# Kernel optimization log

Measured on AMD Instinct MI355X. Metric: run time of the kernel, lower is better.

## Reference

```python
import jax, jax.numpy as jnp
import numpy as np

D_IN = 256
H = 512
DT = 0.01
LN_EPS = 1e-5


def setup_inputs() -> dict:
    key = jax.random.key(0)
    ks = jax.random.split(key, 12)
    def lin(k, fan_in, shape):
        bound = 1.0 / np.sqrt(fan_in)
        return jax.random.uniform(k, shape, jnp.float32, -bound, bound)
    x = jax.random.normal(ks[0], (64, 1024, D_IN), jnp.float32)
    return {
        "x": x,
        # input_mapper: Linear(D_IN+H, 2H)
        "Wm": lin(ks[1], D_IN + H, (D_IN + H, 2 * H)),
        "bm": lin(ks[2], D_IN + H, (2 * H,)),
        # f_theta: Linear(H,H) -> SiLU -> Linear(H,H)
        "Wf1": lin(ks[3], H, (H, H)),
        "bf1": lin(ks[4], H, (H,)),
        "Wf2": lin(ks[5], H, (H, H)),
        "bf2": lin(ks[6], H, (H,)),
        # tau_net: Linear(H,H) -> Softplus
        "Wt": lin(ks[7], H, (H, H)),
        "bt": lin(ks[8], H, (H,)),
        # LayerNorm(H)
        "gamma": jnp.ones((H,), jnp.float32),
        "beta": jnp.zeros((H,), jnp.float32),
    }


def _layernorm(h, gamma, beta):
    mu = jnp.mean(h, axis=-1, keepdims=True)
    var = jnp.var(h, axis=-1, keepdims=True)
    return (h - mu) * jax.lax.rsqrt(var + LN_EPS) * gamma + beta


def reference(x, Wm, bm, Wf1, bf1, Wf2, bf2, Wt, bt, gamma, beta):
    B = x.shape[0]
    h0 = jnp.zeros((B, H), x.dtype)

    def step(h, u_t):
        combined = jnp.concatenate([u_t, h], axis=-1)      # (B, D_IN+H)
        mapped = combined @ Wm + bm                        # (B, 2H)
        g, core = jnp.split(mapped, 2, axis=-1)
        g = jax.nn.sigmoid(g)
        tau = jax.nn.softplus(core @ Wt + bt) + 1e-6       # (B, H)
        z = g * jnp.tanh(core)
        f = jax.nn.silu(z @ Wf1 + bf1) @ Wf2 + bf2         # (B, H)
        h_new = _layernorm(h + (DT / tau) * f, gamma, beta)
        return h_new, h_new

    # scan over time: x (B,T,D) -> (T,B,D)
    _, hs = jax.lax.scan(step, h0, jnp.swapaxes(x, 0, 1))
    return jnp.swapaxes(hs, 0, 1)                          # (B, T, H)
```

## Files before the change

kernel.cpp:

```cpp
#include <hip/hip_runtime.h>
#include <hip/hip_bf16.h>

typedef unsigned int        u32;
typedef unsigned short      u16;
typedef unsigned long long  u64;

#define T_STEPS 1024
#define NTH     1024
#define NSL     8
#define NGRP    32

#define OFF_WM4   0
#define OFF_WT4   786432
#define OFF_WF14  1048576
#define OFF_WF24  1310720
#define OFF_FLAGS 1572864
#define OFF_XC    1576960
#define XC_ZC 0
#define XC_F1 32768
#define XC_V  49152
#define XC_SQ 65536

__device__ __forceinline__ float bf2f(u16 u){
  union { u32 u; float f; } x; x.u = ((u32)u) << 16; return x.f;
}
__device__ __forceinline__ u32 f2bf_bits(float f){
  union { float f; u32 u; } x; x.f = f;
  u32 u = x.u;
  return ((u + 0x7fffu + ((u >> 16) & 1u)) >> 16) & 0xffffu;
}
__device__ __forceinline__ u32 pack2(float lo, float hi){
  return (f2bf_bits(hi) << 16) | f2bf_bits(lo);
}
__device__ __forceinline__ void split2(float f0, float f1, u32& hi, u32& lo){
  u32 b0 = f2bf_bits(f0), b1 = f2bf_bits(f1);
  hi = (b1 << 16) | b0;
  float r0 = f0 - bf2f((u16)b0);
  float r1 = f1 - bf2f((u16)b1);
  lo = pack2(r0, r1);
}
__device__ __forceinline__ float dot2bf(u32 a, u32 b, float c){
  float d;
  asm("v_dot2_f32_bf16 %0, %1, %2, %3" : "=v"(d) : "v"(a), "v"(b), "v"(c));
  return d;
}
__device__ __forceinline__ float sigmoidf_(float x){ return 1.f/(1.f + __expf(-x)); }
__device__ __forceinline__ float tanhf_(float x){ return 1.f - 2.f/(__expf(2.f*x) + 1.f); }
__device__ __forceinline__ float softplusf_(float x){ return (x > 20.f) ? x : log1pf(__expf(x)); }

__device__ __forceinline__ int sniff_bf16(const void* gamma){
  return (((const u32*)gamma)[0] == 0x3F803F80u) ? 1 : 0;
}
__device__ __forceinline__ float ldsc(const void* p, int i, int isbf){
  return isbf ? bf2f(((const u16*)p)[i]) : ((const float*)p)[i];
}
__device__ __forceinline__ float ldwf(const void* p, long i, int isbf){
  return isbf ? bf2f(((const u16*)p)[i]) : ((const float*)p)[i];
}

__device__ __forceinline__ void xst(u64* p, u32 hi, u32 lo){
  u64 v = ((u64)lo << 32) | (u64)hi;
  __hip_atomic_store(p, v, __ATOMIC_RELAXED, __HIP_MEMORY_SCOPE_AGENT);
}
__device__ __forceinline__ void xst64(u64* p, u64 v){
  __hip_atomic_store(p, v, __ATOMIC_RELAXED, __HIP_MEMORY_SCOPE_AGENT);
}
__device__ __forceinline__ u64 xld(const u64* p){
  return __hip_atomic_load(p, __ATOMIC_RELAXED, __HIP_MEMORY_SCOPE_AGENT);
}

__device__ __forceinline__ void groupsync(u32* line, int j, u32 tgt, u32* deadf)
{
  __syncthreads();
  if (threadIdx.x == 0 && *deadf == 0u) {
    __hip_atomic_store(line + j, tgt, __ATOMIC_RELAXED, __HIP_MEMORY_SCOPE_AGENT);
    u32 gu = 0;
    for (;;) {
      u32 mn = 0xffffffffu;
      #pragma unroll
      for (int q = 0; q < NSL; ++q)
        mn = min(mn, __hip_atomic_load(line + q, __ATOMIC_RELAXED, __HIP_MEMORY_SCOPE_AGENT));
      if (mn >= tgt) break;
      if (++gu > 1000000u) { *deadf = 1u; break; }
      if (gu > 64u) __builtin_amdgcn_s_sleep(1);
    }
  }
  __syncthreads();
}

__global__ void repack_kernel(const void* __restrict__ Wm, const void* __restrict__ Wt,
                              const void* __restrict__ Wf1, const void* __restrict__ Wf2,
                              const void* __restrict__ gamma, u32* __restrict__ ws)
{
  if (blockIdx.x < 16)
    __hip_atomic_store(ws + OFF_FLAGS + blockIdx.x*256 + threadIdx.x, 0u,
                       __ATOMIC_RELAXED, __HIP_MEMORY_SCOPE_AGENT);

  const int isbf = sniff_bf16(gamma);
  int i = blockIdx.x * 256 + threadIdx.x;
  if (i < 196608) {
    long k2 = i >> 9, c = i & 511;
    float w00 = ldwf(Wm, (2*k2)*1024 + 2*c,   isbf);
    float w01 = ldwf(Wm, (2*k2)*1024 + 2*c+1, isbf);
    float w10 = ldwf(Wm, (2*k2+1)*1024 + 2*c,   isbf);
    float w11 = ldwf(Wm, (2*k2+1)*1024 + 2*c+1, isbf);
    u32 h0, l0, h1, l1;
    split2(w00, w10, h0, l0);
    split2(w01, w11, h1, l1);
    uint4 v; v.x = h0; v.y = h1; v.z = l0; v.w = l1;
    ((uint4*)(ws + OFF_WM4))[k2*512 + c] = v;
  } else if (i < 327680) {
    int r = i - 196608;
    const void* W = (r < 65536) ? Wt : Wf1;
    u32* dst = ws + ((r < 65536) ? OFF_WT4 : OFF_WF14);
    r &= 65535;
    long k2 = r >> 8, c = r & 255;
    float w00 = ldwf(W, (2*k2)*512 + 2*c,   isbf);
    float w01 = ldwf(W, (2*k2)*512 + 2*c+1, isbf);
    float w10 = ldwf(W, (2*k2+1)*512 + 2*c,   isbf);
    float w11 = ldwf(W, (2*k2+1)*512 + 2*c+1, isbf);
    u32 h0, l0, h1, l1;
    split2(w00, w10, h0, l0);
    split2(w01, w11, h1, l1);
    uint4 v; v.x = h0; v.y = h1; v.z = l0; v.w = l1;
    ((uint4*)dst)[k2*256 + c] = v;
  } else if (i < 458752) {
    int q = i - 327680;
    long k2 = q >> 9, jj = q & 511;
    float w0 = ldwf(Wf2, (2*k2)*512 + jj,   isbf);
    float w1 = ldwf(Wf2, (2*k2+1)*512 + jj, isbf);
    u32 h, l;
    split2(w0, w1, h, l);
    uint2 v; v.x = h; v.y = l;
    ((uint2*)(ws + OFF_WF24))[k2*512 + jj] = v;
  }
}

__global__ __launch_bounds__(NTH, 4) void scan_kernel(
    const void* __restrict__ xv, u32* __restrict__ wsb,
    const void* bm, const void* bf1,
    const void* bf2v, const void* bt,
    const void* gammav, const void* betav,
    void* outv)
{
  __shared__ __align__(16) u64 comb2[2][388];
  __shared__ __align__(16) u64 actAll[2][516];
  __shared__ __align__(16) float2 redB[8][128];
  __shared__ float vAll[2][520];
  __shared__ float hloc[2][66];
  __shared__ float gbuf[2][66], corebuf[2][66], dta2[2][66], vloc[2][66];
  __shared__ float2 sqL[2][8];
  __shared__ float gammaL[512], betaL[512];
  __shared__ float bmL[128], bf1L[64], btL[64], bf2L[64];
  __shared__ u32 deadf;

  const int tid  = threadIdx.x;
  const int wg   = blockIdx.x;
  const int j    = wg & (NSL-1);
  const int g    = wg >> 3;
  const int isbf = sniff_bf16(gammav);

  const uint4* Wm4  = (const uint4*)(wsb + OFF_WM4);
  const uint4* Wt4  = (const uint4*)(wsb + OFF_WT4);
  const uint4* Wf14 = (const uint4*)(wsb + OFF_WF14);
  const uint2* Wf22 = (const uint2*)(wsb + OFF_WF24);
  u32* arr0 = wsb + OFF_FLAGS + (g*3 + 0)*32;
  u32* arr1 = wsb + OFF_FLAGS + (g*3 + 1)*32;
  u32* arr2 = wsb + OFF_FLAGS + (g*3 + 2)*32;
  u64* XC = (u64*)(wsb + OFF_XC);
  u64* ZC = XC + XC_ZC;
  u64* F1 = XC + XC_F1;
  u64* Vx = XC + XC_V;
  u64* SQ = XC + XC_SQ;

  const size_t xesz = isbf ? 2u : 4u;
  const char* xrow0 = (const char*)xv + (size_t)(2*g)   * T_STEPS * 256 * xesz;
  const char* xrow1 = (const char*)xv + (size_t)(2*g+1) * T_STEPS * 256 * xesz;

  if (tid == 0) deadf = 0u;
  if (tid < 512) {
    gammaL[tid] = ldsc(gammav, tid, isbf);
    betaL[tid]  = ldsc(betav, tid, isbf);
    int r = tid >> 8, c2 = tid & 255;
    comb2[r][128 + c2] = 0ull;
  }
  if (tid < 128) {
    int gc = tid >> 6, cc = tid & 63;
    bmL[tid] = ldsc(bm, gc ? (512 + 64*j + cc) : (64*j + cc), isbf);
    hloc[gc][cc] = 0.f;
  }
  if (tid < 64) {
    bf1L[tid] = ldsc(bf1, 64*j + tid, isbf);
    btL[tid]  = ldsc(bt, 64*j + tid, isbf);
    bf2L[tid] = ldsc(bf2v, 64*j + tid, isbf);
  }
  if (tid < 256) {
    int r = tid >> 7, i = tid & 127;
    const char* xr = r ? xrow1 : xrow0;
    if (isbf) comb2[r][i] = (u64)(((const u32*)xr)[i]);
    else {
      float2 f = ((const float2*)xr)[i];
      u32 h, l; split2(f.x, f.y, h, l);
      comb2[r][i] = ((u64)l << 32) | (u64)h;
    }
  }
  __syncthreads();

  for (int t = 0; t < T_STEPS; ++t) {
    {
      const int rB = tid & 1, cp = (tid >> 1) & 31, gc = (tid >> 6) & 1, kq = tid >> 7;
      float a0 = 0.f, a1 = 0.f;
      const uint4* w = Wm4 + (gc ? 256 : 0) + 32*j + cp;
      const int k0 = kq * 48;
      #pragma unroll 8
      for (int k2 = k0; k2 < k0 + 48; ++k2) {
        u64 chl = comb2[rB][k2];
        u32 cH = (u32)chl, cL = (u32)(chl >> 32);
        uint4 wA = w[(size_t)k2 * 512];
        a0 = dot2bf(cH, wA.x, a0); a0 = dot2bf(cH, wA.z, a0); a0 = dot2bf(cL, wA.x, a0);
        a1 = dot2bf(cH, wA.y, a1); a1 = dot2bf(cH, wA.w, a1); a1 = dot2bf(cL, wA.y, a1);
      }
      redB[kq][tid & 127] = make_float2(a0, a1);
    }
    __syncthreads();
    if (tid < 256) {
      float a0 = 0.f, a1 = 0.f;
      #pragma unroll
      for (int q = 0; q < 8; ++q) { float2 s = redB[q][tid & 127]; a0 += s.x; a1 += s.y; }
      int r = tid & 1, cp = (tid >> 1) & 31, gc = (tid >> 6) & 1;
      if (gc == 0) {
        a0 += bmL[2*cp]; a1 += bmL[2*cp+1];
        gbuf[r][2*cp]   = sigmoidf_(a0);
        gbuf[r][2*cp+1] = sigmoidf_(a1);
      } else {
        a0 += bmL[64 + 2*cp]; a1 += bmL[64 + 2*cp+1];
        corebuf[r][2*cp] = a0; corebuf[r][2*cp+1] = a1;
        u32 h, l; split2(a0, a1, h, l);
        xst(ZC + (size_t)g*1024 + r*512 + 256 + 32*j + cp, h, l);
      }
    } else if (tid >= 512 && tid < 768) {
      if (t + 1 < T_STEPS) {
        int idx = tid - 512, r = idx >> 7, i = idx & 127;
        const char* xr = r ? xrow1 : xrow0;
        if (isbf) comb2[r][i] = (u64)(((const u32*)xr)[(t+1)*128 + i]);
        else {
          float2 f = ((const float2*)xr)[(t+1)*128 + i];
          u32 h, l; split2(f.x, f.y, h, l);
          comb2[r][i] = ((u64)l << 32) | (u64)h;
        }
      }
    }
    __syncthreads();
    if (tid < 64) {
      int r = tid >> 5, p = tid & 31;
      float z0 = gbuf[r][2*p]   * tanhf_(corebuf[r][2*p]);
      float z1 = gbuf[r][2*p+1] * tanhf_(corebuf[r][2*p+1]);
      u32 h, l; split2(z0, z1, h, l);
      xst(ZC + (size_t)g*1024 + r*512 + 32*j + p, h, l);
    }
    groupsync(arr0, j, (u32)(t+1), &deadf);

    actAll[tid >> 9][tid & 511] = xld(ZC + (size_t)g*1024 + tid);
    __syncthreads();

    {
      const int rB = tid & 1, cp = (tid >> 1) & 31, sel = (tid >> 6) & 1, kq = tid >> 7;
      const uint4* w = (sel ? Wt4 : Wf14) + 32*j + cp;
      const u64* aP = actAll[rB] + sel*256;
      float d0 = 0.f, d1 = 0.f;
      const int k0 = kq * 32;
      #pragma unroll 8
      for (int k2 = k0; k2 < k0 + 32; ++k2) {
        u64 a = aP[k2];
        u32 aH = (u32)a, aL = (u32)(a >> 32);
        uint4 wA = w[(size_t)k2 * 256];
        d0 = dot2bf(aH, wA.x, d0); d0 = dot2bf(aH, wA.z, d0); d0 = dot2bf(aL, wA.x, d0);
        d1 = dot2bf(aH, wA.y, d1); d1 = dot2bf(aH, wA.w, d1); d1 = dot2bf(aL, wA.y, d1);
      }
      redB[kq][tid & 127] = make_float2(d0, d1);
    }
    __syncthreads();
    if (tid < 256) {
      float d0 = 0.f, d1 = 0.f;
      #pragma unroll
      for (int q = 0; q < 8; ++q) { float2 s = redB[q][tid & 127]; d0 += s.x; d1 += s.y; }
      int r = tid & 1, cp = (tid >> 1) & 31, sel = (tid >> 6) & 1;
      if (sel == 0) {
        d0 += bf1L[2*cp]; d1 += bf1L[2*cp+1];
        float q0 = d0 * sigmoidf_(d0), q1 = d1 * sigmoidf_(d1);
        u32 h, l; split2(q0, q1, h, l);
        xst(F1 + (size_t)g*512 + r*256 + 32*j + cp, h, l);
      } else {
        d0 += btL[2*cp]; d1 += btL[2*cp+1];
        dta2[r][2*cp]   = 0.01f / (softplusf_(d0) + 1e-6f);
        dta2[r][2*cp+1] = 0.01f / (softplusf_(d1) + 1e-6f);
      }
    }
    groupsync(arr1, j, (u32)(t+1), &deadf);

    if (tid < 512) actAll[tid >> 8][tid & 255] = xld(F1 + (size_t)g*512 + tid);
    __syncthreads();

    {
      const int rB = tid & 1, c = (tid >> 1) & 63, kq = tid >> 7;
      const uint2* w = Wf22 + 64*j + c;
      float e = 0.f;
      const int k0 = kq * 32;
      #pragma unroll 8
      for (int k2 = k0; k2 < k0 + 32; ++k2) {
        u64 a = actAll[rB][k2];
        u32 aH = (u32)a, aL = (u32)(a >> 32);
        uint2 wA = w[(size_t)k2 * 512];
        e = dot2bf(aH, wA.x, e); e = dot2bf(aH, wA.y, e); e = dot2bf(aL, wA.x, e);
      }
      redB[kq][tid & 127].x = e;
    }
    __syncthreads();
    if (tid < 128) {
      float e = 0.f;
      #pragma unroll
      for (int q = 0; q < 8; ++q) e += redB[q][tid].x;
      int r = tid & 1, c = tid >> 1;
      float f2v = e + bf2L[c];
      float v = hloc[r][c] + dta2[r][c] * f2v;
      vloc[r][c] = v;
    }
    __syncthreads();
    if (tid < 128) {
      int r = tid >> 6, i = tid & 63;
      float s = vloc[r][i], q = s*s;
      #pragma unroll
      for (int off = 32; off > 0; off >>= 1) {
        s += __shfl_xor(s, off);
        q += __shfl_xor(q, off);
      }
      if (i == 0) {
        union { float2 f; u64 u; } pk; pk.f = make_float2(s, q);
        xst64(SQ + (size_t)g*32 + r*8 + j, pk.u);
      }
    } else if (tid < 192) {
      int idx = tid - 128, r = idx >> 5, p = idx & 31;
      union { float2 f; u64 u; } pk;
      pk.f = make_float2(vloc[r][2*p], vloc[r][2*p+1]);
      xst64(Vx + (size_t)g*512 + r*256 + 32*j + p, pk.u);
    }
    groupsync(arr2, j, (u32)(t+1), &deadf);

    if (tid < 512) {
      int r = tid >> 8, c2 = tid & 255;
      union { float2 f; u64 u; } pk; pk.u = xld(Vx + (size_t)g*512 + tid);
      vAll[r][2*c2] = pk.f.x; vAll[r][2*c2+1] = pk.f.y;
    }
    if (tid < 16) {
      union { float2 f; u64 u; } pk; pk.u = xld(SQ + (size_t)g*32 + tid);
      sqL[tid >> 3][tid & 7] = pk.f;
    }
    __syncthreads();

    if (tid < 512) {
      int r = tid >> 8, c2 = tid & 255;
      float S = 0.f, Q = 0.f;
      #pragma unroll
      for (int q = 0; q < 8; ++q) { S += sqL[r][q].x; Q += sqL[r][q].y; }
      const float mu  = S * (1.f/512.f);
      const float var = Q * (1.f/512.f) - mu*mu;
      const float rs  = rsqrtf(var + 1e-5f);
      int c0 = 2*c2;
      float hn0 = (vAll[r][c0]   - mu) * rs * gammaL[c0]   + betaL[c0];
      float hn1 = (vAll[r][c0+1] - mu) * rs * gammaL[c0+1] + betaL[c0+1];
      u32 h, l; split2(hn0, hn1, h, l);
      comb2[r][128 + c2] = ((u64)l << 32) | (u64)h;
      if ((c2 >> 5) == j) {
        int lc = c2 & 31;
        hloc[r][2*lc]   = hn0;
        hloc[r][2*lc+1] = hn1;
        size_t op = ((size_t)(2*g + r) * T_STEPS + t) * 256 + c2;
        if (isbf) ((u32*)outv)[op] = (f2bf_bits(hn1) << 16) | f2bf_bits(hn0);
        else      ((float2*)outv)[op] = make_float2(hn0, hn1);
      }
    }
    __syncthreads();
  }
}

extern "C" void kernel_launch(void* const* d_in, const int* in_sizes, int n_in,
                              void* d_out, int out_size, void* d_ws, size_t ws_size,
                              hipStream_t stream)
{
  (void)in_sizes; (void)n_in; (void)out_size; (void)ws_size;
  const void* xs   = d_in[0];
  const void* Wm   = d_in[1];
  const void* bm   = d_in[2];
  const void* Wf1  = d_in[3];
  const void* bf1  = d_in[4];
  const void* Wf2  = d_in[5];
  const void* bf2v = d_in[6];
  const void* Wt   = d_in[7];
  const void* bt   = d_in[8];
  const void* gm   = d_in[9];
  const void* bta  = d_in[10];
  u32* ws = (u32*)d_ws;

  repack_kernel<<<1792, 256, 0, stream>>>(Wm, Wt, Wf1, Wf2, gm, ws);
  scan_kernel<<<256, NTH, 0, stream>>>(xs, ws, bm, bf1, bf2v, bt, gm, bta, d_out);
}
```

Measured before the change: 19.39 ms.

## Overlap input-projection matmul with group barriers and pack barrier flags into one word

The x-part of the input-mapper matmul (first 128 k-pairs) is precomputed for the next step during the barrier waits after the z and F1 stages. The barrier is split into arm and wait phases so this independent work fills the spin time. Per-slice flags become bytes in a single 64-bit word polled with one atomic load instead of eight. The gate/tanh epilogue and the LayerNorm statistics are fused to remove intermediate shared buffers and some __syncthreads. The risks are byte-flag wraparound past 255 steps, since the wait compares for equality, and extra register pressure from the carried accumulators.

Result: slower. 20.28 ms (+4.6%).

```diff
diff --git a/kernel.cpp b/kernel.cpp
--- a/kernel.cpp
+++ b/kernel.cpp
@@ -4,6 +4,7 @@
 typedef unsigned int        u32;
 typedef unsigned short      u16;
 typedef unsigned long long  u64;
+typedef unsigned char       u8;
 
 #define T_STEPS 1024
 #define NTH     1024
@@ -68,21 +69,24 @@
 __device__ __forceinline__ u64 xld(const u64* p){
   return __hip_atomic_load(p, __ATOMIC_RELAXED, __HIP_MEMORY_SCOPE_AGENT);
 }
-
-__device__ __forceinline__ void groupsync(u32* line, int j, u32 tgt, u32* deadf)
-{
-  __syncthreads();
+__device__ __forceinline__ void xst32(u32* p, u32 v){
+  __hip_atomic_store(p, v, __ATOMIC_RELAXED, __HIP_MEMORY_SCOPE_AGENT);
+}
+__device__ __forceinline__ u32 xld32(const u32* p){
+  return __hip_atomic_load(p, __ATOMIC_RELAXED, __HIP_MEMORY_SCOPE_AGENT);
+}
+
+__device__ __forceinline__ void gs_arm(u64* lineq, int j, u32 tgt){
+  if (threadIdx.x == 0)
+    __hip_atomic_store((u8*)lineq + j, (u8)tgt, __ATOMIC_RELAXED, __HIP_MEMORY_SCOPE_AGENT);
+}
+__device__ __forceinline__ void gs_wait(u64* lineq, u32 tgt, u32* deadf){
   if (threadIdx.x == 0 && *deadf == 0u) {
-    __hip_atomic_store(line + j, tgt, __ATOMIC_RELAXED, __HIP_MEMORY_SCOPE_AGENT);
+    const u64 pat = 0x0101010101010101ull * (u64)(tgt & 0xFFu);
     u32 gu = 0;
-    for (;;) {
-      u32 mn = 0xffffffffu;
-      #pragma unroll
-      for (int q = 0; q < NSL; ++q)
-        mn = min(mn, __hip_atomic_load(line + q, __ATOMIC_RELAXED, __HIP_MEMORY_SCOPE_AGENT));
-      if (mn >= tgt) break;
+    while (__hip_atomic_load(lineq, __ATOMIC_RELAXED, __HIP_MEMORY_SCOPE_AGENT) != pat) {
       if (++gu > 1000000u) { *deadf = 1u; break; }
-      if (gu > 64u) __builtin_amdgcn_s_sleep(1);
+      if (gu > 256u) __builtin_amdgcn_s_sleep(1);
     }
   }
   __syncthreads();
@@ -148,8 +152,8 @@
   __shared__ __align__(16) float2 redB[8][128];
   __shared__ float vAll[2][520];
   __shared__ float hloc[2][66];
-  __shared__ float gbuf[2][66], corebuf[2][66], dta2[2][66], vloc[2][66];
-  __shared__ float2 sqL[2][8];
+  __shared__ float dta2[2][66];
+  __shared__ float2 sqL[2][16];
   __shared__ float gammaL[512], betaL[512];
   __shared__ float bmL[128], bf1L[64], btL[64], bf2L[64];
   __shared__ u32 deadf;
@@ -164,25 +168,34 @@
   const uint4* Wt4  = (const uint4*)(wsb + OFF_WT4);
   const uint4* Wf14 = (const uint4*)(wsb + OFF_WF14);
   const uint2* Wf22 = (const uint2*)(wsb + OFF_WF24);
-  u32* arr0 = wsb + OFF_FLAGS + (g*3 + 0)*32;
-  u32* arr1 = wsb + OFF_FLAGS + (g*3 + 1)*32;
-  u32* arr2 = wsb + OFF_FLAGS + (g*3 + 2)*32;
+  u64* arr0q = (u64*)(wsb + OFF_FLAGS) + (size_t)(g*3 + 0)*16;
+  u64* arr1q = (u64*)(wsb + OFF_FLAGS) + (size_t)(g*3 + 1)*16;
+  u64* arr2q = (u64*)(wsb + OFF_FLAGS) + (size_t)(g*3 + 2)*16;
   u64* XC = (u64*)(wsb + OFF_XC);
   u64* ZC = XC + XC_ZC;
   u64* F1 = XC + XC_F1;
-  u64* Vx = XC + XC_V;
+  u32* Vxu = (u32*)(XC + XC_V);
   u64* SQ = XC + XC_SQ;
 
   const size_t xesz = isbf ? 2u : 4u;
   const char* xrow0 = (const char*)xv + (size_t)(2*g)   * T_STEPS * 256 * xesz;
   const char* xrow1 = (const char*)xv + (size_t)(2*g+1) * T_STEPS * 256 * xesz;
+
+  const int rB = tid & 1, cpB = (tid >> 1) & 31, gcB = (tid >> 6) & 1, kqB = tid >> 7;
+  const uint4* wB = Wm4 + (gcB ? 256 : 0) + 32*j + cpB;
 
   if (tid == 0) deadf = 0u;
   if (tid < 512) {
     gammaL[tid] = ldsc(gammav, tid, isbf);
     betaL[tid]  = ldsc(betav, tid, isbf);
+  }
+  {
+    int r = tid >> 9, c2 = tid & 255;
+    if ((tid & 511) < 256) comb2[r][128 + c2] = 0ull;
+  }
+  {
     int r = tid >> 8, c2 = tid & 255;
-    comb2[r][128 + c2] = 0ull;
+    if (tid < 512) comb2[r][128 + c2] = 0ull;
   }
   if (tid < 128) {
     int gc = tid >> 6, cc = tid & 63;
@@ -206,38 +219,54 @@
   }
   __syncthreads();
 
+  float uacc0 = 0.f, uacc1 = 0.f;
+  {
+    const int k0 = kqB * 16;
+    #pragma unroll 8
+    for (int k2 = k0; k2 < k0 + 16; ++k2) {
+      u64 chl = comb2[rB][k2];
+      u32 cH = (u32)chl, cL = (u32)(chl >> 32);
+      uint4 wA = wB[(size_t)k2 * 512];
+      uacc0 = dot2bf(cH, wA.x, uacc0); uacc0 = dot2bf(cH, wA.z, uacc0); uacc0 = dot2bf(cL, wA.x, uacc0);
+      uacc1 = dot2bf(cH, wA.y, uacc1); uacc1 = dot2bf(cH, wA.w, uacc1); uacc1 = dot2bf(cL, wA.y, uacc1);
+    }
+  }
+
   for (int t = 0; t < T_STEPS; ++t) {
-    {
-      const int rB = tid & 1, cp = (tid >> 1) & 31, gc = (tid >> 6) & 1, kq = tid >> 7;
-      float a0 = 0.f, a1 = 0.f;
-      const uint4* w = Wm4 + (gc ? 256 : 0) + 32*j + cp;
-      const int k0 = kq * 48;
+    const u32 tgt = (u32)(t + 1);
+
+    {
+      float a0 = uacc0, a1 = uacc1;
+      const int k0 = 128 + kqB * 32;
       #pragma unroll 8
-      for (int k2 = k0; k2 < k0 + 48; ++k2) {
+      for (int k2 = k0; k2 < k0 + 32; ++k2) {
         u64 chl = comb2[rB][k2];
         u32 cH = (u32)chl, cL = (u32)(chl >> 32);
-        uint4 wA = w[(size_t)k2 * 512];
+        uint4 wA = wB[(size_t)k2 * 512];
         a0 = dot2bf(cH, wA.x, a0); a0 = dot2bf(cH, wA.z, a0); a0 = dot2bf(cL, wA.x, a0);
         a1 = dot2bf(cH, wA.y, a1); a1 = dot2bf(cH, wA.w, a1); a1 = dot2bf(cL, wA.y, a1);
       }
-      redB[kq][tid & 127] = make_float2(a0, a1);
-    }
-    __syncthreads();
-    if (tid < 256) {
-      float a0 = 0.f, a1 = 0.f;
+      redB[kqB][tid & 127] = make_float2(a0, a1);
+    }
+    __syncthreads();
+
+    if (tid < 64) {
+      int r = tid & 1, cp = tid >> 1;
+      int ig = r | (cp << 1), ic = ig | 64;
+      float g0 = 0.f, g1 = 0.f, c0 = 0.f, c1 = 0.f;
       #pragma unroll
-      for (int q = 0; q < 8; ++q) { float2 s = redB[q][tid & 127]; a0 += s.x; a1 += s.y; }
-      int r = tid & 1, cp = (tid >> 1) & 31, gc = (tid >> 6) & 1;
-      if (gc == 0) {
-        a0 += bmL[2*cp]; a1 += bmL[2*cp+1];
-        gbuf[r][2*cp]   = sigmoidf_(a0);
-        gbuf[r][2*cp+1] = sigmoidf_(a1);
-      } else {
-        a0 += bmL[64 + 2*cp]; a1 += bmL[64 + 2*cp+1];
-        corebuf[r][2*cp] = a0; corebuf[r][2*cp+1] = a1;
-        u32 h, l; split2(a0, a1, h, l);
-        xst(ZC + (size_t)g*1024 + r*512 + 256 + 32*j + cp, h, l);
-      }
+      for (int q = 0; q < 8; ++q) {
+        float2 sg = redB[q][ig]; g0 += sg.x; g1 += sg.y;
+        float2 sc = redB[q][ic]; c0 += sc.x; c1 += sc.y;
+      }
+      g0 = sigmoidf_(g0 + bmL[2*cp]);  g1 = sigmoidf_(g1 + bmL[2*cp+1]);
+      c0 += bmL[64 + 2*cp];            c1 += bmL[64 + 2*cp+1];
+      float z0 = g0 * tanhf_(c0), z1 = g1 * tanhf_(c1);
+      u32 h, l;
+      split2(c0, c1, h, l);
+      xst(ZC + (size_t)g*1024 + r*512 + 256 + 32*j + cp, h, l);
+      split2(z0, z1, h, l);
+      xst(ZC + (size_t)g*1024 + r*512 + 32*j + cp, h, l);
     } else if (tid >= 512 && tid < 768) {
       if (t + 1 < T_STEPS) {
         int idx = tid - 512, r = idx >> 7, i = idx & 127;
@@ -251,24 +280,32 @@
       }
     }
     __syncthreads();
-    if (tid < 64) {
-      int r = tid >> 5, p = tid & 31;
-      float z0 = gbuf[r][2*p]   * tanhf_(corebuf[r][2*p]);
-      float z1 = gbuf[r][2*p+1] * tanhf_(corebuf[r][2*p+1]);
-      u32 h, l; split2(z0, z1, h, l);
-      xst(ZC + (size_t)g*1024 + r*512 + 32*j + p, h, l);
-    }
-    groupsync(arr0, j, (u32)(t+1), &deadf);
+    gs_arm(arr0q, j, tgt);
+
+    {
+      float a0 = 0.f, a1 = 0.f;
+      const int k0 = kqB * 16;
+      #pragma unroll 8
+      for (int k2 = k0; k2 < k0 + 8; ++k2) {
+        u64 chl = comb2[rB][k2];
+        u32 cH = (u32)chl, cL = (u32)(chl >> 32);
+        uint4 wA = wB[(size_t)k2 * 512];
+        a0 = dot2bf(cH, wA.x, a0); a0 = dot2bf(cH, wA.z, a0); a0 = dot2bf(cL, wA.x, a0);
+        a1 = dot2bf(cH, wA.y, a1); a1 = dot2bf(cH, wA.w, a1); a1 = dot2bf(cL, wA.y, a1);
+      }
+      uacc0 = a0; uacc1 = a1;
+    }
+    gs_wait(arr0q, tgt, &deadf);
 
     actAll[tid >> 9][tid & 511] = xld(ZC + (size_t)g*1024 + tid);
     __syncthreads();
 
     {
-      const int rB = tid & 1, cp = (tid >> 1) & 31, sel = (tid >> 6) & 1, kq = tid >> 7;
-      const uint4* w = (sel ? Wt4 : Wf14) + 32*j + cp;
+      const int sel = gcB;
+      const uint4* w = (sel ? Wt4 : Wf14) + 32*j + cpB;
       const u64* aP = actAll[rB] + sel*256;
       float d0 = 0.f, d1 = 0.f;
-      const int k0 = kq * 32;
+      const int k0 = kqB * 32;
       #pragma unroll 8
       for (int k2 = k0; k2 < k0 + 32; ++k2) {
         u64 a = aP[k2];
@@ -277,13 +314,13 @@
         d0 = dot2bf(aH, wA.x, d0); d0 = dot2bf(aH, wA.z, d0); d0 = dot2bf(aL, wA.x, d0);
         d1 = dot2bf(aH, wA.y, d1); d1 = dot2bf(aH, wA.w, d1); d1 = dot2bf(aL, wA.y, d1);
       }
-      redB[kq][tid & 127] = make_float2(d0, d1);
-    }
-    __syncthreads();
-    if (tid < 256) {
+      redB[kqB][tid & 127] = make_float2(d0, d1);
+    }
+    __syncthreads();
+    if (tid < 128) {
       float d0 = 0.f, d1 = 0.f;
       #pragma unroll
-      for (int q = 0; q < 8; ++q) { float2 s = redB[q][tid & 127]; d0 += s.x; d1 += s.y; }
+      for (int q = 0; q < 8; ++q) { float2 s = redB[q][tid]; d0 += s.x; d1 += s.y; }
       int r = tid & 1, cp = (tid >> 1) & 31, sel = (tid >> 6) & 1;
       if (sel == 0) {
         d0 += bf1L[2*cp]; d1 += bf1L[2*cp+1];
@@ -296,16 +333,32 @@
         dta2[r][2*cp+1] = 0.01f / (softplusf_(d1) + 1e-6f);
       }
     }
-    groupsync(arr1, j, (u32)(t+1), &deadf);
+    __syncthreads();
+    gs_arm(arr1q, j, tgt);
+
+    {
+      float a0 = uacc0, a1 = uacc1;
+      const int k0 = kqB * 16 + 8;
+      #pragma unroll 8
+      for (int k2 = k0; k2 < k0 + 8; ++k2) {
+        u64 chl = comb2[rB][k2];
+        u32 cH = (u32)chl, cL = (u32)(chl >> 32);
+        uint4 wA = wB[(size_t)k2 * 512];
+        a0 = dot2bf(cH, wA.x, a0); a0 = dot2bf(cH, wA.z, a0); a0 = dot2bf(cL, wA.x, a0);
+        a1 = dot2bf(cH, wA.y, a1); a1 = dot2bf(cH, wA.w, a1); a1 = dot2bf(cL, wA.y, a1);
+      }
+      uacc0 = a0; uacc1 = a1;
+    }
+    gs_wait(arr1q, tgt, &deadf);
 
     if (tid < 512) actAll[tid >> 8][tid & 255] = xld(F1 + (size_t)g*512 + tid);
     __syncthreads();
 
     {
-      const int rB = tid & 1, c = (tid >> 1) & 63, kq = tid >> 7;
+      const int c = (tid >> 1) & 63;
       const uint2* w = Wf22 + 64*j + c;
       float e = 0.f;
-      const int k0 = kq * 32;
+      const int k0 = kqB * 32;
       #pragma unroll 8
       for (int k2 = k0; k2 < k0 + 32; ++k2) {
         u64 a = actAll[rB][k2];
@@ -313,47 +366,39 @@
         uint2 wA = w[(size_t)k2 * 512];
         e = dot2bf(aH, wA.x, e); e = dot2bf(aH, wA.y, e); e = dot2bf(aL, wA.x, e);
       }
-      redB[kq][tid & 127].x = e;
+      redB[kqB][tid & 127].x = e;
     }
     __syncthreads();
     if (tid < 128) {
+      int r = tid & 1, c = tid >> 1;
       float e = 0.f;
       #pragma unroll
       for (int q = 0; q < 8; ++q) e += redB[q][tid].x;
-      int r = tid & 1, c = tid >> 1;
-      float f2v = e + bf2L[c];
-      float v = hloc[r][c] + dta2[r][c] * f2v;
-      vloc[r][c] = v;
-    }
-    __syncthreads();
-    if (tid < 128) {
-      int r = tid >> 6, i = tid & 63;
-      float s = vloc[r][i], q = s*s;
+      float v = hloc[r][c] + dta2[r][c] * (e + bf2L[c]);
+      xst32(Vxu + (size_t)g*1024 + r*512 + 64*j + c, __float_as_uint(v));
+      float s = v, qq = v*v;
       #pragma unroll
-      for (int off = 32; off > 0; off >>= 1) {
-        s += __shfl_xor(s, off);
-        q += __shfl_xor(q, off);
-      }
-      if (i == 0) {
-        union { float2 f; u64 u; } pk; pk.f = make_float2(s, q);
-        xst64(SQ + (size_t)g*32 + r*8 + j, pk.u);
-      }
-    } else if (tid < 192) {
-      int idx = tid - 128, r = idx >> 5, p = idx & 31;
-      union { float2 f; u64 u; } pk;
-      pk.f = make_float2(vloc[r][2*p], vloc[r][2*p+1]);
-      xst64(Vx + (size_t)g*512 + r*256 + 32*j + p, pk.u);
-    }
-    groupsync(arr2, j, (u32)(t+1), &deadf);
-
-    if (tid < 512) {
-      int r = tid >> 8, c2 = tid & 255;
-      union { float2 f; u64 u; } pk; pk.u = xld(Vx + (size_t)g*512 + tid);
-      vAll[r][2*c2] = pk.f.x; vAll[r][2*c2+1] = pk.f.y;
-    }
-    if (tid < 16) {
+      for (int off = 2; off <= 32; off <<= 1) {
+        s  += __shfl_xor(s,  off);
+        qq += __shfl_xor(qq, off);
+      }
+      if ((tid & 63) < 2) {
+        int half = tid >> 6;
+        union { float2 f; u64 u; } pk; pk.f = make_float2(s, qq);
+        xst64(SQ + (size_t)g*32 + r*16 + j*2 + half, pk.u);
+      }
+    }
+    __syncthreads();
+    gs_arm(arr2q, j, tgt);
+    gs_wait(arr2q, tgt, &deadf);
+
+    {
+      u32 bits = xld32(Vxu + (size_t)g*1024 + tid);
+      vAll[tid >> 9][tid & 511] = __uint_as_float(bits);
+    }
+    if (tid < 32) {
       union { float2 f; u64 u; } pk; pk.u = xld(SQ + (size_t)g*32 + tid);
-      sqL[tid >> 3][tid & 7] = pk.f;
+      sqL[tid >> 4][tid & 15] = pk.f;
     }
     __syncthreads();
 
@@ -361,7 +406,7 @@
       int r = tid >> 8, c2 = tid & 255;
       float S = 0.f, Q = 0.f;
       #pragma unroll
-      for (int q = 0; q < 8; ++q) { S += sqL[r][q].x; Q += sqL[r][q].y; }
+      for (int q = 0; q < 16; ++q) { S += sqL[r][q].x; Q += sqL[r][q].y; }
       const float mu  = S * (1.f/512.f);
       const float var = Q * (1.f/512.f) - mu*mu;
       const float rs  = rsqrtf(var + 1e-5f);
```
